# Performance work log

Measured on AMD Instinct MI355X. Metric: run time of the kernel, lower is better.

## Reference

```python
import jax, jax.numpy as jnp
import numpy as np

C, DG, DEPTH = 256, 64, 4
DIN, N, DTR, DCONV = 512, 16, 16, 4  # d_inner=2*C, d_state, dt_rank=ceil(C/16), conv kernel
EPS = 1e-5


def _rms(x, w):
    return x * jax.lax.rsqrt(jnp.mean(x * x, axis=-1, keepdims=True) + EPS) * w


def _causal_conv(x, w, b):
    # x: (M, K, DIN); depthwise causal conv, kernel DCONV
    K = x.shape[1]
    xp = jnp.pad(x, ((0, 0), (DCONV - 1, 0), (0, 0)))
    y = b
    for t in range(DCONV):
        y = y + xp[:, t:t + K, :] * w[:, t]
    return y


def _ssm(u, dt, Bs, Cs, A, D):
    # u, dt: (M, K, DIN); Bs, Cs: (M, K, N); A: (DIN, N); D: (DIN,)
    M, K, Din = u.shape

    def step(s, xs):
        u_t, dt_t, b_t, c_t = xs
        dA = jnp.exp(dt_t[..., None] * A)                    # (M, DIN, N)
        s = s * dA + (dt_t * u_t)[..., None] * b_t[:, None, :]
        y = jnp.einsum('mdn,mn->md', s, c_t)
        return s, y

    s0 = jnp.zeros((M, Din, A.shape[1]), u.dtype)
    xs = (u.transpose(1, 0, 2), dt.transpose(1, 0, 2),
          Bs.transpose(1, 0, 2), Cs.transpose(1, 0, 2))
    _, ys = jax.lax.scan(step, s0, xs)
    return ys.transpose(1, 0, 2) + u * D


def _block(x, p):
    # x: (M, K, C) window-token sequences; one multihead Mamba block
    nw, ipw, cw, cb, xpw, dtw, dtb, alog, dp, ow, gw, gb = p
    h = _rms(x, nw)
    xz = h @ ipw.T                                           # (M, K, 2*DIN)
    u, z = jnp.split(xz, 2, axis=-1)
    u = jax.nn.silu(_causal_conv(u, cw, cb))
    dbl = u @ xpw.T                                          # (M, K, DTR+2N)
    dt = jax.nn.softplus(dbl[..., :DTR] @ dtw.T + dtb)
    Bs, Cs = dbl[..., DTR:DTR + N], dbl[..., DTR + N:]
    y = _ssm(u, dt, Bs, Cs, -jnp.exp(alog), dp)
    y = y * jax.nn.silu(z)
    match = x + y @ ow.T                                     # residual
    geom = match @ gw.T + gb
    return match, geom


def setup_inputs() -> dict:
    key = jax.random.key(0)
    ks = jax.random.split(key, 16)
    B, H, W = 1, 48, 48
    f32 = jnp.float32
    nrm = lambda k, s: jax.random.normal(k, s, f32)
    inp = {
        'feat_match_0': nrm(ks[0], (B, C, H, W)),
        'feat_match_1': nrm(ks[1], (B, C, H, W)),
        'feat_geom_0': nrm(ks[2], (B, DG, H, W)),
        'feat_geom_1': nrm(ks[3], (B, DG, H, W)),
        'spans_x_0': jax.random.randint(ks[4], (B, H, W), 0, 11, jnp.int32),
        'spans_y_0': jax.random.randint(ks[5], (B, H, W), 0, 11, jnp.int32),
        'spans_x_1': jax.random.randint(ks[6], (B, H, W), 0, 11, jnp.int32),
        'spans_y_1': jax.random.randint(ks[7], (B, H, W), 0, 11, jnp.int32),
        'norm_w': jnp.ones((DEPTH, C), f32),
        'in_proj_w': 0.02 * nrm(ks[8], (DEPTH, 2 * DIN, C)),
        'conv_w': 0.02 * nrm(ks[9], (DEPTH, DIN, DCONV)),
        'conv_b': jnp.zeros((DEPTH, DIN), f32),
        'xproj_w': 0.02 * nrm(ks[10], (DEPTH, DTR + 2 * N, DIN)),
        'dt_w': 0.02 * nrm(ks[11], (DEPTH, DIN, DTR)),
        'dt_b': jnp.full((DEPTH, DIN), -4.0, f32),
        'A_log': jnp.log(jnp.arange(1, N + 1, dtype=f32)) * jnp.ones((DEPTH, DIN, 1), f32),
        'D_p': jnp.ones((DEPTH, DIN), f32),
        'out_w': 0.02 * nrm(ks[12], (DEPTH, C, DIN)),
        'geom_w': 0.02 * nrm(ks[13], (DEPTH, DG, C)),
        'geom_b': jnp.zeros((DEPTH, DG), f32),
    }
    return inp


def reference(feat_match_0, feat_match_1, feat_geom_0, feat_geom_1,
              spans_x_0, spans_y_0, spans_x_1, spans_y_1,
              norm_w, in_proj_w, conv_w, conv_b, xproj_w, dt_w, dt_b,
              A_log, D_p, out_w, geom_w, geom_b):
    B, Cc, H, W = feat_match_0.shape
    # avg_span is data-dependent but integer-valued -> treated as static (spans are int constants)
    sp = np.concatenate([np.asarray(spans_x_0).ravel(), np.asarray(spans_y_0).ravel()]).astype(np.float64)
    k = max(3, min(int(sp.mean()), 15))
    pad = k // 2
    K = k * k

    def unfold(f):
        fp = jnp.pad(f, ((0, 0), (0, 0), (pad, pad), (pad, pad)))
        pats = jnp.stack([fp[:, :, di:di + H, dj:dj + W]
                          for di in range(k) for dj in range(k)], axis=-1)  # (B,C,H,W,K)
        return pats.transpose(0, 2, 3, 4, 1).reshape(B, H * W, K, Cc)

    # stack both images along batch so all blocks run once
    w = jnp.concatenate([unfold(feat_match_0), unfold(feat_match_1)], axis=0)
    w = w.reshape(2 * B * H * W, K, Cc)

    params = (norm_w, in_proj_w, conv_w, conv_b, xproj_w, dt_w, dt_b,
              A_log, D_p, out_w, geom_w, geom_b)
    match = geom = None
    for i in range(DEPTH):
        p = tuple(a[i] for a in params)
        match, geom = _block(w, p)
        w = match  # dropout is identity at inference

    match = match.reshape(2 * B, H * W, K, Cc).mean(axis=2)
    geom = geom.reshape(2 * B, H * W, K, DG).mean(axis=2)
    match = match.reshape(2 * B, H, W, Cc).transpose(0, 3, 1, 2)
    geom = geom.reshape(2 * B, H, W, DG).transpose(0, 3, 1, 2)
    return (match[:B], match[B:], geom[:B], geom[B:])
```

## Files before the change

kernel.cpp:

```cpp
#include <hip/hip_runtime.h>


#define HW   2304
#define WI   48

typedef __attribute__((ext_vector_type(8))) short short8;
typedef __attribute__((ext_vector_type(4))) float f32x4;

union U8u { short8 s8; unsigned u[4]; unsigned short h[8]; };

static __device__ __forceinline__ float ldbf(const unsigned short* p) {
    return __uint_as_float(((unsigned)(*p)) << 16);
}
static __device__ __forceinline__ unsigned short f2bf(float f) {
    unsigned u = __float_as_uint(f);
    u += 0x7fffu + ((u >> 16) & 1u);
    return (unsigned short)(u >> 16);
}
static __device__ __forceinline__ float softplusf(float x) {
    return (x > 20.f) ? x : __logf(1.f + __expf(x));
}

#define HNA_OFF  0
#define U_OFF    16384
#define XS_OFF   49152
#define DBL_OFF  75552
#define RSTD_OFF 80352
#define SMEM_TOTAL 80480

static __device__ __forceinline__ int chunkIdx(int mt, int ks, int q, int tr) {
    return ((mt * 16 + ks) << 6) + (q << 4) + ((tr + 4 * q + 8 * (ks & 1)) & 15);
}
static __device__ __forceinline__ int uIdx(int t, int d) {
    return chunkIdx(t >> 4, d >> 5, (d >> 3) & 3, t & 15) * 8 + (d & 7);
}

__global__ void k_compute(const int* __restrict__ sx, const int* __restrict__ sy,
                          const float* __restrict__ alog, int* __restrict__ kp) {
    __shared__ int sred[4];
    __shared__ int sflag;
    int tid = threadIdx.x;
    if (tid == 0) sflag = 1;
    __syncthreads();
    int s = 0;
    for (int i = tid; i < HW; i += 256) s += sx[i] + sy[i];
    #pragma unroll
    for (int off = 32; off > 0; off >>= 1) s += __shfl_down(s, off);
    if ((tid & 63) == 0) sred[tid >> 6] = s;

    int ok = 1;
    for (int i = tid; i < 4 * 512 * 16; i += 256) {
        int n = i & 15;
        float ref = __logf((float)(n + 1));
        if (fabsf(alog[i] - ref) > 1e-5f) ok = 0;
    }
    if (!ok) atomicAnd(&sflag, 0);
    __syncthreads();
    if (tid == 0) {
        int tot = sred[0] + sred[1] + sred[2] + sred[3];
        int kk = tot / (2 * HW);
        if (kk < 3) kk = 3;
        if (kk > 15) kk = 15;
        kp[0] = kk;
        kp[1] = sflag;
    }
}

#define N_WUBF  131072
#define N_OWBF  65536
#define N_XPBF  12288
#define N_ANEG4 8192
#define N_FT4   294912
#define PREP_TOTAL (N_WUBF + N_OWBF + N_XPBF + N_ANEG4 + N_FT4)

__global__ void prep(const float* __restrict__ ipw, const float* __restrict__ nw,
                     const float* __restrict__ ow,  const float* __restrict__ xpw,
                     const float* __restrict__ alog,
                     const float* __restrict__ fm0, const float* __restrict__ fm1,
                     unsigned short* __restrict__ Wub, unsigned short* __restrict__ owb,
                     unsigned short* __restrict__ xpb, float* __restrict__ Aneg,
                     float* __restrict__ featT) {
    int idx = blockIdx.x * 256 + threadIdx.x;
    if (idx < N_WUBF) {
        int l = idx >> 15, r = idx & 32767;
        int nt = r >> 9, ks = (r >> 6) & 7, L = r & 63;
        int o = nt * 16 + (L & 15), c0 = ks * 32 + ((L >> 4) & 3) * 8;
        const float* src = ipw + (l * 1024 + o) * 256 + c0;
        const float* nws = nw + l * 256 + c0;
        union { unsigned short h[8]; uint4 u4; } vv;
        #pragma unroll
        for (int j = 0; j < 8; ++j) vv.h[j] = f2bf(src[j] * nws[j]);
        ((uint4*)Wub)[idx] = vv.u4;
    } else if (idx < N_WUBF + N_OWBF) {
        int i2 = idx - N_WUBF;
        int l = i2 >> 14, r = i2 & 16383;
        int nt = r >> 10, ks = (r >> 6) & 15, L = r & 63;
        int c = nt * 16 + (L & 15), d0 = ks * 32 + ((L >> 4) & 3) * 8;
        const float* src = ow + (l * 256 + c) * 512 + d0;
        union { unsigned short h[8]; uint4 u4; } vv;
        #pragma unroll
        for (int j = 0; j < 8; ++j) vv.h[j] = f2bf(src[j]);
        ((uint4*)owb)[i2] = vv.u4;
    } else if (idx < N_WUBF + N_OWBF + N_XPBF) {
        int i3 = idx - (N_WUBF + N_OWBF);
        int l = i3 / 3072, r = i3 - l * 3072;
        int nt = r >> 10, ks = (r >> 6) & 15, L = r & 63;
        int jrow = nt * 16 + (L & 15), d0 = ks * 32 + ((L >> 4) & 3) * 8;
        const float* src = xpw + (l * 48 + jrow) * 512 + d0;
        union { unsigned short h[8]; uint4 u4; } vv;
        #pragma unroll
        for (int j = 0; j < 8; ++j) vv.h[j] = f2bf(src[j]);
        ((uint4*)xpb)[i3] = vv.u4;
    } else if (idx < N_WUBF + N_OWBF + N_XPBF + N_ANEG4) {
        int i4 = (idx - (N_WUBF + N_OWBF + N_XPBF)) * 4;
        float4 a = *(const float4*)(alog + i4);
        float4 o4;
        o4.x = -__expf(a.x); o4.y = -__expf(a.y);
        o4.z = -__expf(a.z); o4.w = -__expf(a.w);
        *(float4*)(Aneg + i4) = o4;
    } else if (idx < PREP_TOTAL) {
        int t = idx - (N_WUBF + N_OWBF + N_XPBF + N_ANEG4);
        int p = t >> 6, c0 = (t & 63) * 4;
        int img = (p >= HW) ? 1 : 0;
        int pix = p - img * HW;
        const float* fm = img ? fm1 : fm0;
        float4 o4;
        o4.x = fm[(c0 + 0) * HW + pix];
        o4.y = fm[(c0 + 1) * HW + pix];
        o4.z = fm[(c0 + 2) * HW + pix];
        o4.w = fm[(c0 + 3) * HW + pix];
        *(float4*)(featT + p * 256 + c0) = o4;
    }
}

template <int K, int KS>
static __device__ void block_run(
    char* __restrict__ smem, int aflag,
    const float* __restrict__ conv_w, const float* __restrict__ conv_b,
    const float* __restrict__ dtw, const float* __restrict__ dt_b,
    const float* __restrict__ Aneg, const float* __restrict__ D_p,
    const float* __restrict__ geom_w, const float* __restrict__ geom_b,
    const unsigned short* __restrict__ Wub, const unsigned short* __restrict__ owb,
    const unsigned short* __restrict__ xpb, const float* __restrict__ featT,
    float* __restrict__ outp) {

    constexpr int MT = (K + 15) / 16;
    constexpr int PAD = KS / 2;
    const int tid = threadIdx.x;
    const int lane = tid & 63;
    const int w = tid >> 6;
    const int m = blockIdx.x;
    const int img = m / HW;
    const int pix = m - img * HW;
    const int pi = pix / WI;
    const int pj = pix - pi * WI;

    float* xs = (float*)(smem + XS_OFF);
    unsigned short* us = (unsigned short*)(smem + U_OFF);
    short8* hnA = (short8*)(smem + HNA_OFF);
    float* dbl = (float*)(smem + DBL_OFF);
    float* rstd = (float*)(smem + RSTD_OFF);
    const short8* U8 = (const short8*)us;
    short8* us8w = (short8*)us;
    const short8* Wub8 = (const short8*)Wub;
    const short8* owb8 = (const short8*)owb;
    const short8* xpb8 = (const short8*)xpb;
    const f32x4 z4 = {0.f, 0.f, 0.f, 0.f};

    {
        const float* ft = featT + img * (HW * 256);
        int c = tid & 255;
        for (int t = (tid >> 8); t < K; t += 2) {
            int di = t / KS, dj = t - di * KS;
            int r = pi + di - PAD, cc = pj + dj - PAD;
            float v = 0.f;
            if (r >= 0 && r < WI && cc >= 0 && cc < WI)
                v = ft[(r * WI + cc) * 256 + c];
            xs[t * 264 + c] = v;
        }
    }
    __syncthreads();

    for (int l = 0; l < 4; ++l) {
        for (int t = w; t < K; t += 8) {
            float s = 0.f;
            #pragma unroll
            for (int q = 0; q < 4; ++q) {
                float v = xs[t * 264 + lane + 64 * q];
                s += v * v;
            }
            #pragma unroll
            for (int off = 32; off > 0; off >>= 1) s += __shfl_down(s, off);
            if (lane == 0) rstd[t] = rsqrtf(s * (1.f / 256.f) + 1e-5f);
        }
        __syncthreads();

        for (int f = tid; f < MT * 8 * 64; f += 512) {
            int mt = f >> 9;
            int ks = (f >> 6) & 7, L = f & 63;
            int mm = mt * 16 + (L & 15);
            int c0 = ks * 32 + ((L >> 4) & 3) * 8;
            U8u vv;
            if (mm < K) {
                float rs = rstd[mm];
                const float4* xr = (const float4*)(xs + mm * 264 + c0);
                float4 xa = xr[0], xb = xr[1];
                vv.h[0] = f2bf(xa.x * rs); vv.h[1] = f2bf(xa.y * rs);
                vv.h[2] = f2bf(xa.z * rs); vv.h[3] = f2bf(xa.w * rs);
                vv.h[4] = f2bf(xb.x * rs); vv.h[5] = f2bf(xb.y * rs);
                vv.h[6] = f2bf(xb.z * rs); vv.h[7] = f2bf(xb.w * rs);
            } else {
                #pragma unroll
                for (int j = 0; j < 8; ++j) vv.h[j] = 0;
            }
            hnA[f] = vv.s8;
        }
        __syncthreads();

        {
            const short8* WB = Wub8 + l * 32768;
            f32x4 acc[4][MT];
            #pragma unroll
            for (int c = 0; c < 4; ++c)
                #pragma unroll
                for (int mt = 0; mt < MT; ++mt) acc[c][mt] = z4;
            short8 bcur[4];
            #pragma unroll
            for (int c = 0; c < 4; ++c) bcur[c] = WB[((w * 4 + c) * 8) * 64 + lane];
            #pragma unroll
            for (int ks = 0; ks < 8; ++ks) {
                short8 av[MT];
                #pragma unroll
                for (int mt = 0; mt < MT; ++mt) av[mt] = hnA[(mt * 8 + ks) * 64 + lane];
                short8 bn[4];
                if (ks < 7) {
                    #pragma unroll
                    for (int c = 0; c < 4; ++c) bn[c] = WB[((w * 4 + c) * 8 + ks + 1) * 64 + lane];
                }
                #pragma unroll
                for (int c = 0; c < 4; ++c)
                    #pragma unroll
                    for (int mt = 0; mt < MT; ++mt)
                        acc[c][mt] = __builtin_amdgcn_mfma_f32_16x16x32_bf16(av[mt], bcur[c], acc[c][mt], 0, 0, 0);
                if (ks < 7) {
                    #pragma unroll
                    for (int c = 0; c < 4; ++c) bcur[c] = bn[c];
                }
            }
            int r0 = (lane >> 4) << 2, col = lane & 15;
            #pragma unroll
            for (int c = 0; c < 4; ++c) {
                int d = (w * 4 + c) * 16 + col;
                #pragma unroll
                for (int mt = 0; mt < MT; ++mt)
                    #pragma unroll
                    for (int r = 0; r < 4; ++r)
                        us[uIdx(mt * 16 + r0 + r, d)] = f2bf(acc[c][mt][r]);
            }
        }
        __syncthreads();

        {
            const float* cwL = conv_w + l * 2048;
            const float* cbL = conv_b + l * 512;
            int rr = tid & 7, qq = (tid >> 3) & 3, kk = tid >> 5;
            int d0 = kk * 32 + qq * 8;
            float4 wv[8]; float bias[8];
            #pragma unroll
            for (int j = 0; j < 8; ++j) wv[j] = *(const float4*)(cwL + (d0 + j) * 4);
            #pragma unroll
            for (int j = 0; j < 8; j += 4) {
                float4 b4 = *(const float4*)(cbL + d0 + j);
                bias[j] = b4.x; bias[j + 1] = b4.y; bias[j + 2] = b4.z; bias[j + 3] = b4.w;
            }
            constexpr int NT = (K + 7) / 8;
            U8u outb[NT];
            #pragma unroll
            for (int i = 0; i < NT; ++i) {
                int t = rr + 8 * i;
                if (t < K) {
                    float y[8];
                    #pragma unroll
                    for (int j = 0; j < 8; ++j) y[j] = bias[j];
                    #pragma unroll
                    for (int dl = 0; dl < 4; ++dl) {
                        int ts = t - dl;
                        if (ts >= 0) {
                            U8u uu; uu.s8 = U8[chunkIdx(ts >> 4, kk, qq, ts & 15)];
                            #pragma unroll
                            for (int j = 0; j < 8; ++j) {
                                float uv = __uint_as_float(((unsigned)uu.h[j]) << 16);
                                float wc = (dl == 0) ? wv[j].w : (dl == 1) ? wv[j].z
                                         : (dl == 2) ? wv[j].y : wv[j].x;
                                y[j] += wc * uv;
                            }
                        }
                    }
                    #pragma unroll
                    for (int j = 0; j < 8; ++j) {
                        float a = y[j];
                        outb[i].h[j] = f2bf(a / (1.f + __expf(-a)));
                    }
                }
            }
            __syncthreads();
            #pragma unroll
            for (int i = 0; i < NT; ++i) {
                int t = rr + 8 * i;
                if (t < K)
                    us8w[chunkIdx(t >> 4, kk, qq, t & 15)] = outb[i].s8;
            }
        }
        __syncthreads();

        if (w < 3 * MT) {
            const short8* XB = xpb8 + l * 3072;
            int nt = w / MT, mt = w % MT;
            f32x4 acc = z4;
            #pragma unroll
            for (int ks = 0; ks < 16; ++ks) {
                short8 av = U8[chunkIdx(mt, ks, lane >> 4, lane & 15)];
                short8 b = XB[(nt * 16 + ks) * 64 + lane];
                acc = __builtin_amdgcn_mfma_f32_16x16x32_bf16(av, b, acc, 0, 0, 0);
            }
            int r0 = (lane >> 4) << 2, col = lane & 15;
            #pragma unroll
            for (int r = 0; r < 4; ++r) {
                int t = mt * 16 + r0 + r;
                if (t < K) dbl[t * 48 + nt * 16 + col] = acc[r];
            }
        }
        __syncthreads();

        {
            const float* An  = Aneg + l * 8192 + tid * 16;
            const float* dtp = dtw  + l * 8192 + tid * 16;
            float Av[16], tw[16];
            #pragma unroll
            for (int n = 0; n < 16; n += 4) {
                float4 b = *(const float4*)(dtp + n);
                tw[n] = b.x; tw[n + 1] = b.y; tw[n + 2] = b.z; tw[n + 3] = b.w;
            }
            if (!aflag) {
                #pragma unroll
                for (int n = 0; n < 16; n += 4) {
                    float4 a = *(const float4*)(An + n);
                    Av[n] = a.x; Av[n + 1] = a.y; Av[n + 2] = a.z; Av[n + 3] = a.w;
                }
            }
            float dtb0 = dt_b[l * 512 + tid];
            float Dv = D_p[l * 512 + tid];
            float s[16];
            #pragma unroll
            for (int n = 0; n < 16; ++n) s[n] = 0.f;
            for (int t = 0; t < K; ++t) {
                const float4* db4 = (const float4*)(dbl + t * 48);
                float4 t0 = db4[0], t1 = db4[1], t2 = db4[2], t3 = db4[3];
                float dta = dtb0
                    + t0.x * tw[0]  + t0.y * tw[1]  + t0.z * tw[2]  + t0.w * tw[3]
                    + t1.x * tw[4]  + t1.y * tw[5]  + t1.z * tw[6]  + t1.w * tw[7]
                    + t2.x * tw[8]  + t2.y * tw[9]  + t2.z * tw[10] + t2.w * tw[11]
                    + t3.x * tw[12] + t3.y * tw[13] + t3.z * tw[14] + t3.w * tw[15];
                float dt0 = softplusf(dta);
                float u = ldbf(us + uIdx(t, tid));
                float du = dt0 * u;
                float y = u * Dv;
                float dA[16];
                if (aflag) {
                    float e1 = __expf(-dt0);
                    float p = e1;
                    dA[0] = p;
                    #pragma unroll
                    for (int n = 1; n < 16; ++n) { p *= e1; dA[n] = p; }
                } else {
                    #pragma unroll
                    for (int n = 0; n < 16; ++n) dA[n] = __expf(dt0 * Av[n]);
                }
                #pragma unroll
                for (int g = 0; g < 4; ++g) {
                    float4 Bg = db4[4 + g], Cg = db4[8 + g];
                    s[4*g+0] = s[4*g+0] * dA[4*g+0] + du * Bg.x; y += s[4*g+0] * Cg.x;
                    s[4*g+1] = s[4*g+1] * dA[4*g+1] + du * Bg.y; y += s[4*g+1] * Cg.y;
                    s[4*g+2] = s[4*g+2] * dA[4*g+2] + du * Bg.z; y += s[4*g+2] * Cg.z;
                    s[4*g+3] = s[4*g+3] * dA[4*g+3] + du * Bg.w; y += s[4*g+3] * Cg.w;
                }
                us[uIdx(t, tid)] = f2bf(y);
            }
        }
        __syncthreads();

        {
            const short8* WB = Wub8 + l * 32768;
            f32x4 acc[4][MT];
            #pragma unroll
            for (int c = 0; c < 4; ++c)
                #pragma unroll
                for (int mt = 0; mt < MT; ++mt) acc[c][mt] = z4;
            short8 bcur[4];
            #pragma unroll
            for (int c = 0; c < 4; ++c) bcur[c] = WB[((32 + w * 4 + c) * 8) * 64 + lane];
            #pragma unroll
            for (int ks = 0; ks < 8; ++ks) {
                short8 av[MT];
                #pragma unroll
                for (int mt = 0; mt < MT; ++mt) av[mt] = hnA[(mt * 8 + ks) * 64 + lane];
                short8 bn[4];
                if (ks < 7) {
                    #pragma unroll
                    for (int c = 0; c < 4; ++c) bn[c] = WB[((32 + w * 4 + c) * 8 + ks + 1) * 64 + lane];
                }
                #pragma unroll
                for (int c = 0; c < 4; ++c)
                    #pragma unroll
                    for (int mt = 0; mt < MT; ++mt)
                        acc[c][mt] = __builtin_amdgcn_mfma_f32_16x16x32_bf16(av[mt], bcur[c], acc[c][mt], 0, 0, 0);
                if (ks < 7) {
                    #pragma unroll
                    for (int c = 0; c < 4; ++c) bcur[c] = bn[c];
                }
            }
            int r0 = (lane >> 4) << 2, col = lane & 15;
            #pragma unroll
            for (int c = 0; c < 4; ++c) {
                int d = (w * 4 + c) * 16 + col;
                #pragma unroll
                for (int mt = 0; mt < MT; ++mt)
                    #pragma unroll
                    for (int r = 0; r < 4; ++r) {
                        int idx = uIdx(mt * 16 + r0 + r, d);
                        float z = acc[c][mt][r];
                        float g = z / (1.f + __expf(-z));
                        us[idx] = f2bf(ldbf(us + idx) * g);
                    }
            }
        }
        __syncthreads();

        {
            const short8* OB = owb8 + l * 16384;
            f32x4 acc[2][MT];
            #pragma unroll
            for (int c = 0; c < 2; ++c)
                #pragma unroll
                for (int mt = 0; mt < MT; ++mt) acc[c][mt] = z4;
            #pragma unroll
            for (int ks = 0; ks < 16; ++ks) {
                short8 av[MT];
                #pragma unroll
                for (int mt = 0; mt < MT; ++mt)
                    av[mt] = U8[chunkIdx(mt, ks, lane >> 4, lane & 15)];
                #pragma unroll
                for (int c = 0; c < 2; ++c) {
                    short8 b = OB[((w * 2 + c) * 16 + ks) * 64 + lane];
                    #pragma unroll
                    for (int mt = 0; mt < MT; ++mt)
                        acc[c][mt] = __builtin_amdgcn_mfma_f32_16x16x32_bf16(av[mt], b, acc[c][mt], 0, 0, 0);
                }
            }
            int r0 = (lane >> 4) << 2, col = lane & 15;
            #pragma unroll
            for (int c = 0; c < 2; ++c) {
                int cc = (w * 2 + c) * 16 + col;
                #pragma unroll
                for (int mt = 0; mt < MT; ++mt)
                    #pragma unroll
                    for (int r = 0; r < 4; ++r) {
                        int t = mt * 16 + r0 + r;
                        if (t < K) xs[t * 264 + cc] += acc[c][mt][r];
                    }
            }
        }
        __syncthreads();
    }

    float* mm = dbl;
    if (tid < 256) {
        float ssum = 0.f;
        #pragma unroll
        for (int t = 0; t < K; ++t) ssum += xs[t * 264 + tid];
        float mv = ssum * (1.f / (float)K);
        mm[tid] = mv;
        outp[(img * 256 + tid) * HW + pix] = mv;
    }
    __syncthreads();
    {
        int row = tid >> 3, sub = tid & 7;
        const float* gwp = geom_w + 3 * (64 * 256) + row * 256 + sub * 32;
        const float* mmp = mm + sub * 32;
        float acc = 0.f;
        #pragma unroll
        for (int c = 0; c < 32; ++c) acc += mmp[c] * gwp[c];
        acc += __shfl_down(acc, 4);
        acc += __shfl_down(acc, 2);
        acc += __shfl_down(acc, 1);
        if (sub == 0)
            outp[2 * 256 * HW + img * (64 * HW) + row * HW + pix] = acc + geom_b[3 * 64 + row];
    }
}

__global__ __launch_bounds__(512, 4) void mamba_main(
    const float* __restrict__ conv_w, const float* __restrict__ conv_b,
    const float* __restrict__ dtw, const float* __restrict__ dt_b,
    const float* __restrict__ Aneg, const float* __restrict__ D_p,
    const float* __restrict__ geom_w, const float* __restrict__ geom_b,
    const unsigned short* __restrict__ Wub, const unsigned short* __restrict__ owb,
    const unsigned short* __restrict__ xpb, const float* __restrict__ featT,
    const int* __restrict__ kp, float* __restrict__ outp) {
    extern __shared__ __align__(16) char smem[];
    int k = kp[0];
    int aflag = kp[1];
    if (k <= 3)
        block_run<9, 3>(smem, aflag, conv_w, conv_b, dtw, dt_b, Aneg, D_p, geom_w,
                        geom_b, Wub, owb, xpb, featT, outp);
    else if (k == 4)
        block_run<16, 4>(smem, aflag, conv_w, conv_b, dtw, dt_b, Aneg, D_p, geom_w,
                         geom_b, Wub, owb, xpb, featT, outp);
    else
        block_run<25, 5>(smem, aflag, conv_w, conv_b, dtw, dt_b, Aneg, D_p, geom_w,
                         geom_b, Wub, owb, xpb, featT, outp);
}

extern "C" void kernel_launch(void* const* d_in, const int* in_sizes, int n_in,
                              void* d_out, int out_size, void* d_ws, size_t ws_size,
                              hipStream_t stream) {
    const float* fm0    = (const float*)d_in[0];
    const float* fm1    = (const float*)d_in[1];
    const int*   sx0    = (const int*)d_in[4];
    const int*   sy0    = (const int*)d_in[5];
    const float* norm_w = (const float*)d_in[8];
    const float* ipw    = (const float*)d_in[9];
    const float* conv_w = (const float*)d_in[10];
    const float* conv_b = (const float*)d_in[11];
    const float* xpw    = (const float*)d_in[12];
    const float* dtw    = (const float*)d_in[13];
    const float* dtb    = (const float*)d_in[14];
    const float* alog   = (const float*)d_in[15];
    const float* dp     = (const float*)d_in[16];
    const float* ow     = (const float*)d_in[17];
    const float* gw     = (const float*)d_in[18];
    const float* gb     = (const float*)d_in[19];

    char* wsb = (char*)d_ws;
    int* kp              = (int*)wsb;
    unsigned short* Wub  = (unsigned short*)(wsb + 256);
    unsigned short* owb  = (unsigned short*)(wsb + 2097408);
    unsigned short* xpb  = (unsigned short*)(wsb + 3145984);
    float* Aneg          = (float*)(wsb + 3342592);
    float* featT         = (float*)(wsb + 3473664);

    hipFuncSetAttribute(reinterpret_cast<const void*>(&mamba_main),
                        hipFuncAttributeMaxDynamicSharedMemorySize, SMEM_TOTAL);

    k_compute<<<1, 256, 0, stream>>>(sx0, sy0, alog, kp);
    prep<<<(PREP_TOTAL + 255) / 256, 256, 0, stream>>>(ipw, norm_w, ow, xpw, alog,
                                                       fm0, fm1, Wub, owb, xpb,
                                                       Aneg, featT);
    mamba_main<<<4608, 512, SMEM_TOTAL, stream>>>(conv_w, conv_b, dtw, dtb, Aneg, dp,
                                                  gw, gb, Wub, owb, xpb, featT, kp,
                                                  (float*)d_out);
}
```

Baseline: 1.844 ms.

## Fuse causal conv and SiLU into in_proj MFMA epilogue via cross-lane shuffles

The depthwise causal conv plus SiLU is now computed straight from the in_proj MFMA accumulators. Shuffles fetch the previous three time rows from neighbouring lanes and the previous m-tile, so the pre-conv u values are never written to LDS, reread, and synced. This drops a shared-memory round trip and at least two barriers per layer, at the cost of extra shuffles and register pressure. The z-gating epilogue now skips padded rows, and the launch bounds are changed to pin waves per EU at 4.

```diff
diff --git a/kernel.cpp b/kernel.cpp
--- a/kernel.cpp
+++ b/kernel.cpp
@@ -161,7 +161,6 @@
     float* dbl = (float*)(smem + DBL_OFF);
     float* rstd = (float*)(smem + RSTD_OFF);
     const short8* U8 = (const short8*)us;
-    short8* us8w = (short8*)us;
     const short8* Wub8 = (const short8*)Wub;
     const short8* owb8 = (const short8*)owb;
     const short8* xpb8 = (const short8*)xpb;
@@ -219,6 +218,8 @@
 
         {
             const short8* WB = Wub8 + l * 32768;
+            const float* cwL = conv_w + l * 2048;
+            const float* cbL = conv_b + l * 512;
             f32x4 acc[4][MT];
             #pragma unroll
             for (int c = 0; c < 4; ++c)
@@ -247,68 +248,47 @@
                     for (int c = 0; c < 4; ++c) bcur[c] = bn[c];
                 }
             }
-            int r0 = (lane >> 4) << 2, col = lane & 15;
+            int g = lane >> 4, col = lane & 15;
             #pragma unroll
             for (int c = 0; c < 4; ++c) {
                 int d = (w * 4 + c) * 16 + col;
-                #pragma unroll
-                for (int mt = 0; mt < MT; ++mt)
-                    #pragma unroll
-                    for (int r = 0; r < 4; ++r)
-                        us[uIdx(mt * 16 + r0 + r, d)] = f2bf(acc[c][mt][r]);
-            }
-        }
-        __syncthreads();
-
-        {
-            const float* cwL = conv_w + l * 2048;
-            const float* cbL = conv_b + l * 512;
-            int rr = tid & 7, qq = (tid >> 3) & 3, kk = tid >> 5;
-            int d0 = kk * 32 + qq * 8;
-            float4 wv[8]; float bias[8];
-            #pragma unroll
-            for (int j = 0; j < 8; ++j) wv[j] = *(const float4*)(cwL + (d0 + j) * 4);
-            #pragma unroll
-            for (int j = 0; j < 8; j += 4) {
-                float4 b4 = *(const float4*)(cbL + d0 + j);
-                bias[j] = b4.x; bias[j + 1] = b4.y; bias[j + 2] = b4.z; bias[j + 3] = b4.w;
-            }
-            constexpr int NT = (K + 7) / 8;
-            U8u outb[NT];
-            #pragma unroll
-            for (int i = 0; i < NT; ++i) {
-                int t = rr + 8 * i;
-                if (t < K) {
-                    float y[8];
-                    #pragma unroll
-                    for (int j = 0; j < 8; ++j) y[j] = bias[j];
-                    #pragma unroll
-                    for (int dl = 0; dl < 4; ++dl) {
-                        int ts = t - dl;
-                        if (ts >= 0) {
-                            U8u uu; uu.s8 = U8[chunkIdx(ts >> 4, kk, qq, ts & 15)];
-                            #pragma unroll
-                            for (int j = 0; j < 8; ++j) {
-                                float uv = __uint_as_float(((unsigned)uu.h[j]) << 16);
-                                float wc = (dl == 0) ? wv[j].w : (dl == 1) ? wv[j].z
-                                         : (dl == 2) ? wv[j].y : wv[j].x;
-                                y[j] += wc * uv;
-                            }
+                float4 w4 = *(const float4*)(cwL + d * 4);
+                float bias = cbL[d];
+                float below1[MT], below2[MT], below3[MT];
+                #pragma unroll
+                for (int mt = 0; mt < MT; ++mt) {
+                    float b1 = __shfl_up(acc[c][mt][1], 16);
+                    float b2 = __shfl_up(acc[c][mt][2], 16);
+                    float b3 = __shfl_up(acc[c][mt][3], 16);
+                    float c1 = 0.f, c2 = 0.f, c3 = 0.f;
+                    if (mt >= 1) {
+                        c1 = __shfl(acc[c][mt - 1][1], col + 48);
+                        c2 = __shfl(acc[c][mt - 1][2], col + 48);
+                        c3 = __shfl(acc[c][mt - 1][3], col + 48);
+                    }
+                    below1[mt] = (g == 0) ? c1 : b1;
+                    below2[mt] = (g == 0) ? c2 : b2;
+                    below3[mt] = (g == 0) ? c3 : b3;
+                }
+                #pragma unroll
+                for (int mt = 0; mt < MT; ++mt) {
+                    float a0 = acc[c][mt][0], a1 = acc[c][mt][1];
+                    float a2 = acc[c][mt][2], a3 = acc[c][mt][3];
+                    float cur[4] = { a0, a1, a2, a3 };
+                    float p1[4] = { below3[mt], a0, a1, a2 };
+                    float p2[4] = { below2[mt], below3[mt], a0, a1 };
+                    float p3[4] = { below1[mt], below2[mt], below3[mt], a0 };
+                    #pragma unroll
+                    for (int r = 0; r < 4; ++r) {
+                        int t = mt * 16 + 4 * g + r;
+                        if (t < K) {
+                            float v = bias + w4.w * cur[r] + w4.z * p1[r]
+                                    + w4.y * p2[r] + w4.x * p3[r];
+                            float uo = v / (1.f + __expf(-v));
+                            us[uIdx(t, d)] = f2bf(uo);
                         }
                     }
-                    #pragma unroll
-                    for (int j = 0; j < 8; ++j) {
-                        float a = y[j];
-                        outb[i].h[j] = f2bf(a / (1.f + __expf(-a)));
-                    }
-                }
-            }
-            __syncthreads();
-            #pragma unroll
-            for (int i = 0; i < NT; ++i) {
-                int t = rr + 8 * i;
-                if (t < K)
-                    us8w[chunkIdx(t >> 4, kk, qq, t & 15)] = outb[i].s8;
+                }
             }
         }
         __syncthreads();
@@ -427,10 +407,13 @@
                 for (int mt = 0; mt < MT; ++mt)
                     #pragma unroll
                     for (int r = 0; r < 4; ++r) {
-                        int idx = uIdx(mt * 16 + r0 + r, d);
-                        float z = acc[c][mt][r];
-                        float g = z / (1.f + __expf(-z));
-                        us[idx] = f2bf(ldbf(us + idx) * g);
+                        int t = mt * 16 + r0 + r;
+                        if (t < K) {
+                            int idx = uIdx(t, d);
+                            float z = acc[c][mt][r];
+                            float g = z / (1.f + __expf(-z));
+                            us[idx] = f2bf(ldbf(us + idx) * g);
+                        }
                     }
             }
         }
@@ -498,7 +481,9 @@
     }
 }
 
-__global__ __launch_bounds__(512, 4) void mamba_main(
+__global__ __launch_bounds__(512)
+__attribute__((amdgpu_waves_per_eu(4, 4)))
+void mamba_main(
     const float* __restrict__ conv_w, const float* __restrict__ conv_b,
     const float* __restrict__ dtw, const float* __restrict__ dt_b,
     const float* __restrict__ Aneg, const float* __restrict__ D_p,
```

Measured after the change: 1.635 ms. 11.4% less time.
